# Performance work log

Measured on AMD Instinct MI355X. Metric: run time of the kernel, lower is better.

## Reference

```python
import jax, jax.numpy as jnp
import numpy as np

N_EMBD = 1024
N_HEAD = 16
HEAD_DIM = N_EMBD // N_HEAD  # 64; scale = sqrt(64) = 8


def setup_inputs() -> dict:
    key = jax.random.key(0)
    k0, k1, k2, k3, k4 = jax.random.split(key, 5)
    B, T = 4, 2048
    x = jax.random.normal(k0, (B, T, N_EMBD), dtype=jnp.float32)
    # torch Linear weights are (out,in); we store (in,out) so y = x @ W + b
    W_attn = jax.random.normal(k1, (N_EMBD, 3 * N_EMBD), dtype=jnp.float32) * 0.02
    b_attn = jax.random.normal(k2, (3 * N_EMBD,), dtype=jnp.float32) * 0.02
    W_proj = jax.random.normal(k3, (N_EMBD, N_EMBD), dtype=jnp.float32) * 0.02
    b_proj = jax.random.normal(k4, (N_EMBD,), dtype=jnp.float32) * 0.02
    return {"x": x, "W_attn": W_attn, "b_attn": b_attn,
            "W_proj": W_proj, "b_proj": b_proj}


def reference(x, W_attn, b_attn, W_proj, b_proj):
    B, T, D = x.shape
    scale = 1.0 / np.float32(np.sqrt(HEAD_DIM))
    qkv = x @ W_attn + b_attn                      # [B,T,3D]
    q, k, v = jnp.split(qkv, 3, axis=-1)           # each [B,T,D]
    att = jnp.einsum('bid,bjd->bij', q, k) * scale # [B,T,T]
    causal = jnp.tril(jnp.ones((T, T), dtype=bool))
    att = jnp.where(causal[None, :, :], att, jnp.float32(-jnp.inf))
    att = jax.nn.softmax(att, axis=-1)
    y = jnp.einsum('bij,bjd->bid', att, v)         # [B,T,D]
    return y @ W_proj + b_proj
```

## Files before the change

### kernel.cpp

```cpp
#include <hip/hip_runtime.h>

typedef __attribute__((ext_vector_type(8))) short short8;
typedef __attribute__((ext_vector_type(4))) float f32x4;
typedef __attribute__((ext_vector_type(4))) unsigned short ushort4v;

struct DB0 { static constexpr int value = 0; };
struct DB1 { static constexpr int value = 1; };

__device__ __forceinline__ unsigned short f2bf(float f) {
  unsigned int u = __float_as_uint(f);
  u += 0x7fffu + ((u >> 16) & 1u);
  return (unsigned short)(u >> 16);
}
__device__ __forceinline__ float bf2f(unsigned short h) {
  return __uint_as_float(((unsigned int)h) << 16);
}

__device__ __forceinline__ void gload16(const unsigned short* g, unsigned short* l) {
  __builtin_amdgcn_global_load_lds(
      (const __attribute__((address_space(1))) unsigned int*)g,
      (__attribute__((address_space(3))) unsigned int*)l,
      16, 0, 0);
}

template <int OFF>
__device__ __forceinline__ short8 dsr(unsigned a) {
  short8 r;
  asm volatile("ds_read_b128 %0, %1 offset:%2" : "=v"(r) : "v"(a), "n"(OFF));
  return r;
}

__device__ __forceinline__ void bar() {
  asm volatile("" ::: "memory");
  __builtin_amdgcn_s_barrier();
  asm volatile("" ::: "memory");
}

__global__ __launch_bounds__(256) void conv_x_kernel(const float* __restrict__ x,
                                                     unsigned short* __restrict__ xb) {
  int i = blockIdx.x * 256 + threadIdx.x;
  f32x4 v = ((const f32x4*)x)[i];
  ushort4v o;
  o[0] = f2bf(v[0]); o[1] = f2bf(v[1]); o[2] = f2bf(v[2]); o[3] = f2bf(v[3]);
  ((ushort4v*)xb)[i] = o;
}

__global__ __launch_bounds__(256) void transpose_w_kernel(const float* __restrict__ W,
                                                          unsigned short* __restrict__ Wt,
                                                          int K, int N) {
  __shared__ float tile[32][33];
  int n0 = blockIdx.x * 32, k0 = blockIdx.y * 32;
  int tx = threadIdx.x, ty = threadIdx.y;
#pragma unroll
  for (int j = 0; j < 32; j += 8)
    tile[ty + j][tx] = W[(size_t)(k0 + ty + j) * N + n0 + tx];
  __syncthreads();
#pragma unroll
  for (int j = 0; j < 32; j += 8)
    Wt[(size_t)(n0 + ty + j) * K + k0 + tx] = f2bf(tile[tx][ty + j]);
}

__global__ __launch_bounds__(256) void transpose_v_kernel(const unsigned short* __restrict__ qkv,
                                                          unsigned short* __restrict__ vt) {
  __shared__ unsigned short tile[32][33];
  int b = blockIdx.z;
  int key0 = blockIdx.x * 32, d0 = blockIdx.y * 32;
  int tx = threadIdx.x, ty = threadIdx.y;
#pragma unroll
  for (int j = 0; j < 32; j += 8)
    tile[ty + j][tx] = qkv[(size_t)(b * 2048 + key0 + ty + j) * 3072 + 2048 + d0 + tx];
  __syncthreads();
#pragma unroll
  for (int j = 0; j < 32; j += 8)
    vt[(size_t)(b * 1024 + d0 + ty + j) * 2048 + key0 + tx] = tile[tx][ty + j];
}

__global__ __launch_bounds__(256) void softmax_kernel(unsigned short* __restrict__ S) {
  int row = blockIdx.x * 4 + (threadIdx.x >> 6);
  int l = threadIdx.x & 63;
  unsigned short* p = S + (size_t)row * 2048;
  float v[32];
#pragma unroll
  for (int i = 0; i < 4; i++) {
    short8 raw = *(const short8*)&p[(i * 64 + l) * 8];
#pragma unroll
    for (int j = 0; j < 8; j++) v[i * 8 + j] = bf2f((unsigned short)raw[j]);
  }
  float mx = -3e38f;
#pragma unroll
  for (int i = 0; i < 32; i++) mx = fmaxf(mx, v[i]);
#pragma unroll
  for (int off = 1; off < 64; off <<= 1) mx = fmaxf(mx, __shfl_xor(mx, off));
  float s = 0.f;
#pragma unroll
  for (int i = 0; i < 32; i++) { v[i] = exp2f((v[i] - mx) * 1.44269504f); s += v[i]; }
#pragma unroll
  for (int off = 1; off < 64; off <<= 1) s += __shfl_xor(s, off);
  float inv = 1.f / s;
#pragma unroll
  for (int i = 0; i < 4; i++) {
    short8 o;
#pragma unroll
    for (int j = 0; j < 8; j++) o[j] = (short)f2bf(v[i * 8 + j] * inv);
    *(short8*)&p[(i * 64 + l) * 8] = o;
  }
}

template <int OUTBF>
__global__ __launch_bounds__(256) void gemm128_kernel(
    const unsigned short* __restrict__ A, int lda, long long saz,
    const unsigned short* __restrict__ Bt, int ldb, long long sbz,
    void* __restrict__ Cv, int ldc, long long scz,
    const float* __restrict__ bias, int K, float scale, int causal) {
  __shared__ __align__(16) unsigned short lds[2][16384];

  const int m0 = blockIdx.y * 128, n0 = blockIdx.x * 128;
  const int z = blockIdx.z;
  A += (size_t)z * saz;
  Bt += (size_t)z * sbz;

  const int t = threadIdx.x;
  const int lane = t & 63, wid = t >> 6;
  const int g = lane >> 4, q = lane & 15;
  const int wm = wid >> 1, wn = wid & 1;

  int NT = K >> 6;
  if (causal == 1) { if (n0 >= m0 + 128) NT = 0; }
  else if (causal == 2) { NT = min(K, m0 + 128) >> 6; }

  f32x4 acc[4][4] = {};

  if (NT > 0) {
    const int scol = ((t & 7) * 8) ^ ((t & 32) >> 1);
    const unsigned short* aS = A + (size_t)(m0 + (t >> 3)) * lda + scol;
    const unsigned short* bS = Bt + (size_t)(n0 + (t >> 3)) * ldb + scol;

    auto stage = [&](int tt) {
      unsigned short* d = &lds[tt & 1][wid * 512];
      const unsigned short* sa = aS + (size_t)tt * 64;
      const unsigned short* sb = bS + (size_t)tt * 64;
      gload16(sa, d);
      gload16(sa + (size_t)32 * lda, d + 2048);
      gload16(sa + (size_t)64 * lda, d + 4096);
      gload16(sa + (size_t)96 * lda, d + 6144);
      gload16(sb, d + 8192);
      gload16(sb + (size_t)32 * ldb, d + 10240);
      gload16(sb + (size_t)64 * ldb, d + 12288);
      gload16(sb + (size_t)96 * ldb, d + 14336);
    };

    const unsigned base =
        (unsigned)(unsigned long long)(__attribute__((address_space(3))) unsigned short*)&lds[0][0];
    const int colA = (g * 16) ^ ((q & 4) << 3);
    const unsigned aaB = base + (unsigned)((wm * 64 + q) * 128 + colA);
    const unsigned bbB = base + 16384u + (unsigned)((wn * 64 + q) * 128 + colA);

    stage(0);
    asm volatile("s_waitcnt vmcnt(0)" ::: "memory");
    bar();

    auto body = [&](auto dbc, int tt) {
      constexpr int DB = decltype(dbc)::value;
      const unsigned aa = aaB + DB * 32768u;
      const unsigned bb = bbB + DB * 32768u;
      if (tt + 1 < NT) stage(tt + 1);
      short8 aq[4][2], bq[4][2];
#pragma unroll
      for (int m = 0; m < 4; m++) {
        aq[m][0] = dsr<0>(aa + m * 2048u);
        aq[m][1] = dsr<64>(aa + m * 2048u);
      }
#pragma unroll
      for (int n = 0; n < 4; n++) {
        bq[n][0] = dsr<0>(bb + n * 2048u);
        bq[n][1] = dsr<64>(bb + n * 2048u);
      }
      asm volatile("s_waitcnt lgkmcnt(0)" ::: "memory");
      __builtin_amdgcn_sched_barrier(0);
      __builtin_amdgcn_s_setprio(1);
#pragma unroll
      for (int ks = 0; ks < 2; ks++)
#pragma unroll
        for (int m = 0; m < 4; m++)
#pragma unroll
          for (int n = 0; n < 4; n++)
            acc[m][n] = __builtin_amdgcn_mfma_f32_16x16x32_bf16(aq[m][ks], bq[n][ks], acc[m][n], 0, 0, 0);
      __builtin_amdgcn_s_setprio(0);
      __builtin_amdgcn_sched_barrier(0);
      asm volatile("s_waitcnt vmcnt(0)" ::: "memory");
      bar();
    };

    int tt = 0;
    for (; tt + 2 <= NT; tt += 2) {
      body(DB0{}, tt);
      body(DB1{}, tt + 1);
    }
    if (tt < NT) body(DB0{}, tt);
  }

#pragma unroll
  for (int n = 0; n < 4; n++) {
    int colg = n0 + wn * 64 + n * 16 + q;
    float bv = bias ? bias[colg] : 0.f;
#pragma unroll
    for (int m = 0; m < 4; m++) {
      int rowb = m0 + wm * 64 + m * 16 + g * 4;
#pragma unroll
      for (int r = 0; r < 4; r++) {
        float val = acc[m][n][r] * scale + bv;
        if (causal == 1 && colg > rowb + r) val = -1e30f;
        if (OUTBF) {
          ((unsigned short*)Cv)[(size_t)z * scz + (size_t)(rowb + r) * ldc + colg] = f2bf(val);
        } else {
          ((float*)Cv)[(size_t)z * scz + (size_t)(rowb + r) * ldc + colg] = val;
        }
      }
    }
  }
}

extern "C" void kernel_launch(void* const* d_in, const int* in_sizes, int n_in,
                              void* d_out, int out_size, void* d_ws, size_t ws_size,
                              hipStream_t stream) {
  const float* x  = (const float*)d_in[0];
  const float* Wa = (const float*)d_in[1];
  const float* ba = (const float*)d_in[2];
  const float* Wp = (const float*)d_in[3];
  const float* bp = (const float*)d_in[4];
  float* out = (float*)d_out;

  char* ws = (char*)d_ws;
  unsigned short* qkv = (unsigned short*)(ws);
  unsigned short* xb  = (unsigned short*)(ws + 50331648);
  unsigned short* vt  = (unsigned short*)(ws + 50331648);
  unsigned short* wta = (unsigned short*)(ws + 67108864);
  unsigned short* S   = (unsigned short*)(ws + 73400320);
  unsigned short* y   = (unsigned short*)(ws + 106954752);
  unsigned short* wtp = (unsigned short*)(ws + 123731968);

  conv_x_kernel<<<8192, 256, 0, stream>>>(x, xb);
  transpose_w_kernel<<<dim3(96, 32), dim3(32, 8), 0, stream>>>(Wa, wta, 1024, 3072);
  transpose_w_kernel<<<dim3(32, 32), dim3(32, 8), 0, stream>>>(Wp, wtp, 1024, 1024);

  gemm128_kernel<1><<<dim3(24, 64, 1), 256, 0, stream>>>(
      xb, 1024, 0, wta, 1024, 0, qkv, 3072, 0, ba, 1024, 1.0f, 0);

  gemm128_kernel<1><<<dim3(16, 16, 4), 256, 0, stream>>>(
      qkv, 3072, 2048LL * 3072, qkv + 1024, 3072, 2048LL * 3072,
      S, 2048, 2048LL * 2048, nullptr, 1024, 0.125f, 1);

  softmax_kernel<<<2048, 256, 0, stream>>>(S);

  transpose_v_kernel<<<dim3(64, 32, 4), dim3(32, 8), 0, stream>>>(qkv, vt);

  gemm128_kernel<1><<<dim3(8, 16, 4), 256, 0, stream>>>(
      S, 2048, 2048LL * 2048, vt, 2048, 1024LL * 2048,
      y, 1024, 2048LL * 1024, nullptr, 2048, 1.0f, 2);

  gemm128_kernel<0><<<dim3(8, 64, 1), 256, 0, stream>>>(
      y, 1024, 0, wtp, 1024, 0, out, 1024, 0, bp, 1024, 1.0f, 0);
}
```

Measured before the change: 204.6 us.

## Launch only lower-triangular QK tiles, skip masked softmax columns, remap blocks, reswizzle LDS

The QK^T GEMM now launches only the 136 lower-triangular 128x128 tiles per batch and maps the linear block id to a (row, col) tile with a triangular-number inverse. The softmax reads and writes only up to the end of the row's causal tile, so fully masked column tiles are never touched. Upper tiles of S are left unwritten, which is safe because the PV GEMM stops reading at the causal bound. All GEMMs also reorder block ids for an XCD-aware mapping and use a wider XOR swizzle on LDS columns to cut bank conflicts.

```diff
diff --git a/kernel.cpp b/kernel.cpp
--- a/kernel.cpp
+++ b/kernel.cpp
@@ -78,17 +78,26 @@
 __global__ __launch_bounds__(256) void softmax_kernel(unsigned short* __restrict__ S) {
   int row = blockIdx.x * 4 + (threadIdx.x >> 6);
   int l = threadIdx.x & 63;
+  int rl = row & 2047;
+  int rend = ((rl >> 7) + 1) << 7;
   unsigned short* p = S + (size_t)row * 2048;
   float v[32];
+  float mx = -3e38f;
 #pragma unroll
   for (int i = 0; i < 4; i++) {
-    short8 raw = *(const short8*)&p[(i * 64 + l) * 8];
-#pragma unroll
-    for (int j = 0; j < 8; j++) v[i * 8 + j] = bf2f((unsigned short)raw[j]);
-  }
-  float mx = -3e38f;
-#pragma unroll
-  for (int i = 0; i < 32; i++) mx = fmaxf(mx, v[i]);
+    int c0 = (i * 64 + l) * 8;
+    if (c0 < rend) {
+      short8 raw = *(const short8*)&p[c0];
+#pragma unroll
+      for (int j = 0; j < 8; j++) {
+        v[i * 8 + j] = bf2f((unsigned short)raw[j]);
+        mx = fmaxf(mx, v[i * 8 + j]);
+      }
+    } else {
+#pragma unroll
+      for (int j = 0; j < 8; j++) v[i * 8 + j] = -3e38f;
+    }
+  }
 #pragma unroll
   for (int off = 1; off < 64; off <<= 1) mx = fmaxf(mx, __shfl_xor(mx, off));
   float s = 0.f;
@@ -99,10 +108,13 @@
   float inv = 1.f / s;
 #pragma unroll
   for (int i = 0; i < 4; i++) {
-    short8 o;
-#pragma unroll
-    for (int j = 0; j < 8; j++) o[j] = (short)f2bf(v[i * 8 + j] * inv);
-    *(short8*)&p[(i * 64 + l) * 8] = o;
+    int c0 = (i * 64 + l) * 8;
+    if (c0 < rend) {
+      short8 o;
+#pragma unroll
+      for (int j = 0; j < 8; j++) o[j] = (short)f2bf(v[i * 8 + j] * inv);
+      *(short8*)&p[c0] = o;
+    }
   }
 }
 
@@ -114,8 +126,27 @@
     const float* __restrict__ bias, int K, float scale, int causal) {
   __shared__ __align__(16) unsigned short lds[2][16384];
 
-  const int m0 = blockIdx.y * 128, n0 = blockIdx.x * 128;
-  const int z = blockIdx.z;
+  int bx, by, z;
+  if (causal == 3) {
+    int n = gridDim.x;
+    int i = blockIdx.x;
+    if ((n & 7) == 0) i = (i & 7) * (n >> 3) + (i >> 3);
+    by = (int)((sqrtf(8.f * i + 1.f) - 1.f) * 0.5f);
+    while ((by + 1) * (by + 2) / 2 <= i) by++;
+    while (by * (by + 1) / 2 > i) by--;
+    bx = i - by * (by + 1) / 2;
+    z = blockIdx.y;
+  } else {
+    bx = blockIdx.x; by = blockIdx.y; z = blockIdx.z;
+    int gx = gridDim.x, n = gx * gridDim.y;
+    if ((n & 7) == 0) {
+      int id = by * gx + bx;
+      id = (id & 7) * (n >> 3) + (id >> 3);
+      bx = id % gx;
+      by = id / gx;
+    }
+  }
+  const int m0 = by * 128, n0 = bx * 128;
   A += (size_t)z * saz;
   Bt += (size_t)z * sbz;
 
@@ -131,7 +162,7 @@
   f32x4 acc[4][4] = {};
 
   if (NT > 0) {
-    const int scol = ((t & 7) * 8) ^ ((t & 32) >> 1);
+    const int scol = ((t & 7) * 8) ^ (((t >> 3) & 7) << 3);
     const unsigned short* aS = A + (size_t)(m0 + (t >> 3)) * lda + scol;
     const unsigned short* bS = Bt + (size_t)(n0 + (t >> 3)) * ldb + scol;
 
@@ -151,9 +182,13 @@
 
     const unsigned base =
         (unsigned)(unsigned long long)(__attribute__((address_space(3))) unsigned short*)&lds[0][0];
-    const int colA = (g * 16) ^ ((q & 4) << 3);
-    const unsigned aaB = base + (unsigned)((wm * 64 + q) * 128 + colA);
-    const unsigned bbB = base + 16384u + (unsigned)((wn * 64 + q) * 128 + colA);
+    const int W = (q & 7) << 4;
+    const int colA0 = (g * 16) ^ W;
+    const int colA1 = colA0 ^ 64;
+    const unsigned aa0B = base + (unsigned)((wm * 64 + q) * 128 + colA0);
+    const unsigned aa1B = base + (unsigned)((wm * 64 + q) * 128 + colA1);
+    const unsigned bb0B = base + 16384u + (unsigned)((wn * 64 + q) * 128 + colA0);
+    const unsigned bb1B = base + 16384u + (unsigned)((wn * 64 + q) * 128 + colA1);
 
     stage(0);
     asm volatile("s_waitcnt vmcnt(0)" ::: "memory");
@@ -161,20 +196,18 @@
 
     auto body = [&](auto dbc, int tt) {
       constexpr int DB = decltype(dbc)::value;
-      const unsigned aa = aaB + DB * 32768u;
-      const unsigned bb = bbB + DB * 32768u;
+      const unsigned aa0 = aa0B + DB * 32768u, aa1 = aa1B + DB * 32768u;
+      const unsigned bb0 = bb0B + DB * 32768u, bb1 = bb1B + DB * 32768u;
       if (tt + 1 < NT) stage(tt + 1);
       short8 aq[4][2], bq[4][2];
-#pragma unroll
-      for (int m = 0; m < 4; m++) {
-        aq[m][0] = dsr<0>(aa + m * 2048u);
-        aq[m][1] = dsr<64>(aa + m * 2048u);
-      }
-#pragma unroll
-      for (int n = 0; n < 4; n++) {
-        bq[n][0] = dsr<0>(bb + n * 2048u);
-        bq[n][1] = dsr<64>(bb + n * 2048u);
-      }
+      aq[0][0] = dsr<0>(aa0);    aq[0][1] = dsr<0>(aa1);
+      aq[1][0] = dsr<2048>(aa0); aq[1][1] = dsr<2048>(aa1);
+      aq[2][0] = dsr<4096>(aa0); aq[2][1] = dsr<4096>(aa1);
+      aq[3][0] = dsr<6144>(aa0); aq[3][1] = dsr<6144>(aa1);
+      bq[0][0] = dsr<0>(bb0);    bq[0][1] = dsr<0>(bb1);
+      bq[1][0] = dsr<2048>(bb0); bq[1][1] = dsr<2048>(bb1);
+      bq[2][0] = dsr<4096>(bb0); bq[2][1] = dsr<4096>(bb1);
+      bq[3][0] = dsr<6144>(bb0); bq[3][1] = dsr<6144>(bb1);
       asm volatile("s_waitcnt lgkmcnt(0)" ::: "memory");
       __builtin_amdgcn_sched_barrier(0);
       __builtin_amdgcn_s_setprio(1);
@@ -199,6 +232,7 @@
     if (tt < NT) body(DB0{}, tt);
   }
 
+  const bool maskC = (causal == 1) || (causal == 3);
 #pragma unroll
   for (int n = 0; n < 4; n++) {
     int colg = n0 + wn * 64 + n * 16 + q;
@@ -209,7 +243,7 @@
 #pragma unroll
       for (int r = 0; r < 4; r++) {
         float val = acc[m][n][r] * scale + bv;
-        if (causal == 1 && colg > rowb + r) val = -1e30f;
+        if (maskC && colg > rowb + r) val = -1e30f;
         if (OUTBF) {
           ((unsigned short*)Cv)[(size_t)z * scz + (size_t)(rowb + r) * ldc + colg] = f2bf(val);
         } else {
@@ -246,9 +280,9 @@
   gemm128_kernel<1><<<dim3(24, 64, 1), 256, 0, stream>>>(
       xb, 1024, 0, wta, 1024, 0, qkv, 3072, 0, ba, 1024, 1.0f, 0);
 
-  gemm128_kernel<1><<<dim3(16, 16, 4), 256, 0, stream>>>(
+  gemm128_kernel<1><<<dim3(136, 4), 256, 0, stream>>>(
       qkv, 3072, 2048LL * 3072, qkv + 1024, 3072, 2048LL * 3072,
-      S, 2048, 2048LL * 2048, nullptr, 1024, 0.125f, 1);
+      S, 2048, 2048LL * 2048, nullptr, 1024, 0.125f, 3);
 
   softmax_kernel<<<2048, 256, 0, stream>>>(S);
 
```

Result: no change. 205.2 us (+0.3%).
